# Kernel optimization log

Measured on AMD Instinct MI355X. Metric: run time of the kernel, lower is better.

The kernel has to match this reference:

```python
import jax, jax.numpy as jnp
import numpy as np

B, C, H, W = 8, 96, 56, 56
N = H * W
K = 9
COUT = 2 * C  # 192


def setup_inputs() -> dict:
    key = jax.random.key(0)
    ks = jax.random.split(key, 12)
    s = 0.05
    inp = {
        "x": jax.random.normal(ks[0], (B, C, H, W), jnp.float32),
        "kmap_w": jax.random.normal(ks[1], (C, 500), jnp.float32) * s,
        "kmap_b": jnp.zeros((500,), jnp.float32),
        "kfc_w": jax.random.normal(ks[2], (500, 64), jnp.float32) * s,
        "kfc_b": jnp.zeros((64,), jnp.float32),
        "kmu_w": jax.random.normal(ks[3], (64, 32), jnp.float32) * s,
        "kmu_b": jnp.zeros((32,), jnp.float32),
        "kdec_w": jax.random.normal(ks[4], (32, K), jnp.float32) * s,
        "kdec_b": jnp.zeros((K,), jnp.float32),
        "ec1_w": jax.random.normal(ks[5], (2 * C, C), jnp.float32) * s,
        "ec1_b": jnp.zeros((C,), jnp.float32),
        "ec2_w": jax.random.normal(ks[6], (2 * C, C), jnp.float32) * s,
        "ec2_b": jnp.zeros((C,), jnp.float32),
        "fc_w": jax.random.normal(ks[7], (C, COUT), jnp.float32) * s,
        "fc_b": jnp.zeros((COUT,), jnp.float32),
        "io_w": jax.random.normal(ks[8], (C, COUT), jnp.float32) * s,
        "io_b": jnp.zeros((COUT,), jnp.float32),
        "up_w": jax.random.normal(ks[9], (2 * COUT, COUT), jnp.float32) * s,
        "up_b": jnp.zeros((COUT,), jnp.float32),
    }
    return inp


def reference(x, kmap_w, kmap_b, kfc_w, kfc_b, kmu_w, kmu_b, kdec_w, kdec_b,
              ec1_w, ec1_b, ec2_w, ec2_b, fc_w, fc_b, io_w, io_b, up_w, up_b):
    b, c, h, w = x.shape
    n = h * w
    xf = x.reshape(b, c, n).transpose(0, 2, 1)  # [B, N, C]

    # ---- dense kNN graph (dilation=1, deterministic) ----
    sq = jnp.sum(xf * xf, axis=-1)  # [B, N]
    dist = sq[:, :, None] - 2.0 * jnp.einsum('bnc,bmc->bnm', xf, xf) + sq[:, None, :]
    _, nn_idx = jax.lax.top_k(-dist, K)  # [B, N, K] local neighbor indices

    nodes = xf.reshape(b * n, c)  # flat node features

    # ---- VAE-like K predictor -> per-node kept-degree (non-differentiable) ----
    hK = nodes @ kmap_w + kmap_b
    hK = jax.nn.relu(hK @ kfc_w + kfc_b)
    mu = hK @ kmu_w + kmu_b
    logits = mu @ kdec_w + kdec_b  # [B*N, K]
    k_int = jnp.argmax(logits, axis=1)  # in [0, K-1]

    # edge mask: keep first k_int[i] of node i's K edges
    edge_mask = (jnp.arange(K)[None, :] < k_int[:, None]).reshape(-1)  # [B*N*K]
    emask = edge_mask.astype(nodes.dtype)[:, None]

    # flatten edges with per-batch node offsets (local -> global indices)
    offs = (jnp.arange(b) * n)[:, None, None]
    src = (nn_idx + offs).reshape(-1)              # x_j
    dst = jnp.repeat(jnp.arange(b * n), K)         # x_i (center)

    def edge_conv(feat, wgt, bias):
        xi = feat[dst]
        xj = feat[src]
        msg = jnp.concatenate([xi, xj - xi], axis=-1) @ wgt + bias
        msg = msg * emask  # pruned edges contribute 0 to 'add' aggregation
        return jax.ops.segment_sum(msg, dst, num_segments=b * n)

    h1 = jax.nn.relu(edge_conv(nodes, ec1_w, ec1_b))
    h2 = edge_conv(h1, ec2_w, ec2_b)
    agg = h2 @ fc_w + fc_b                 # EdgeAgg output [B*N, COUT]

    xio = nodes @ io_w + io_b              # inOutFC
    upd = jax.nn.relu(jnp.concatenate([xio, agg], axis=-1) @ up_w + up_b)

    out = upd.reshape(b, n, 2 * c).transpose(0, 2, 1).reshape(b, 2 * c, h, w)
    return out
```

## Files before the change

### kernel.cpp

```cpp
#include <hip/hip_runtime.h>

#define NODES 25088
#define NB 8
#define NPB 3136
#define C 96
#define KNN 9
#define COUT 192
#define MSPLIT 4
#define T12 12
#define NCAND (MSPLIT * T12)

typedef float f32x4 __attribute__((ext_vector_type(4)));
typedef float f32x16 __attribute__((ext_vector_type(16)));
typedef short s16x8 __attribute__((ext_vector_type(8)));

__device__ __forceinline__ unsigned short f2bf(float x) {
  unsigned u = __float_as_uint(x);
  return (unsigned short)((u + 0x7fffu + ((u >> 16) & 1u)) >> 16);
}
__device__ __forceinline__ float bf2f(unsigned short h) {
  return __uint_as_float(((unsigned)h) << 16);
}

__global__ void transpose_kernel(const float* __restrict__ x, float* __restrict__ xf) {
  __shared__ float t[32][33];
  int b = blockIdx.z, ct = blockIdx.y, nt = blockIdx.x;
  int tx = threadIdx.x, ty = threadIdx.y;
  int n0 = nt * 32, c0 = ct * 32;
  const float* xb = x + (size_t)b * C * NPB;
#pragma unroll
  for (int i = 0; i < 4; i++) {
    int c = c0 + ty + i * 8;
    t[ty + i * 8][tx] = xb[(size_t)c * NPB + n0 + tx];
  }
  __syncthreads();
  float* xfb = xf + (size_t)b * NPB * C;
#pragma unroll
  for (int i = 0; i < 4; i++) {
    int n = n0 + ty + i * 8;
    xfb[(size_t)n * C + c0 + tx] = t[tx][ty + i * 8];
  }
}

__global__ void sqsplit_kernel(const float* __restrict__ xf, float* __restrict__ sq,
                               unsigned short* __restrict__ xh,
                               unsigned short* __restrict__ xl) {
  int node = blockIdx.x * 256 + threadIdx.x;
  const float4* r = (const float4*)(xf + (size_t)node * C);
  ushort4* hp = (ushort4*)(xh + (size_t)node * C);
  ushort4* lp = (ushort4*)(xl + (size_t)node * C);
  float s = 0.f;
#pragma unroll
  for (int i = 0; i < 24; i++) {
    float4 v = r[i];
    s += v.x * v.x + v.y * v.y + v.z * v.z + v.w * v.w;
    ushort4 h, l;
    h.x = f2bf(v.x); l.x = f2bf(v.x - bf2f(h.x));
    h.y = f2bf(v.y); l.y = f2bf(v.y - bf2f(h.y));
    h.z = f2bf(v.z); l.z = f2bf(v.z - bf2f(h.z));
    h.w = f2bf(v.w); l.w = f2bf(v.w - bf2f(h.w));
    hp[i] = h;
    lp[i] = l;
  }
  sq[node] = s;
}

__global__ void fold_all_kernel(
    const float* __restrict__ kmap_w, const float* __restrict__ kmap_b,
    const float* __restrict__ kfc_w, const float* __restrict__ kfc_b,
    const float* __restrict__ kmu_w, const float* __restrict__ kmu_b,
    const float* __restrict__ kdec_w, const float* __restrict__ kdec_b,
    const float* __restrict__ ec1_w, const float* __restrict__ ec2_w,
    const float* __restrict__ io_w, const float* __restrict__ io_b,
    const float* __restrict__ fc_w, const float* __restrict__ fc_b,
    const float* __restrict__ up_w, const float* __restrict__ up_b,
    float* __restrict__ WkP, float* __restrict__ bkP, float* __restrict__ WdP,
    float* __restrict__ bdP, float* __restrict__ bPf,
    unsigned short* __restrict__ B1h, unsigned short* __restrict__ B1l,
    unsigned short* __restrict__ B2h, unsigned short* __restrict__ B2l,
    unsigned short* __restrict__ BFh, unsigned short* __restrict__ BFl) {
  __shared__ float sh[4][64];
  int bid = blockIdx.x, tid = threadIdx.x;
  int tx = tid & 63, ty = tid >> 6;
  if (bid < 96) {
    int m = bid;
    float acc = 0.f;
    for (int k = ty; k < 500; k += 4) acc += kmap_w[m * 500 + k] * kfc_w[k * 64 + tx];
    sh[ty][tx] = acc;
    __syncthreads();
    if (ty == 0) WkP[m * 64 + tx] = sh[0][tx] + sh[1][tx] + sh[2][tx] + sh[3][tx];
  } else if (bid == 96) {
    float acc = 0.f;
    for (int k = ty; k < 500; k += 4) acc += kmap_b[k] * kfc_w[k * 64 + tx];
    sh[ty][tx] = acc;
    __syncthreads();
    if (ty == 0) bkP[tx] = sh[0][tx] + sh[1][tx] + sh[2][tx] + sh[3][tx] + kfc_b[tx];
  } else if (bid < 161) {
    int m = bid - 97;
    float acc = 0.f;
    if (tx < 9) {
      for (int k = ty; k < 32; k += 4) acc += kmu_w[m * 32 + k] * kdec_w[k * 9 + tx];
    }
    sh[ty][tx] = acc;
    __syncthreads();
    if (ty == 0 && tx < 9) WdP[m * 9 + tx] = sh[0][tx] + sh[1][tx] + sh[2][tx] + sh[3][tx];
  } else if (bid == 161) {
    float acc = 0.f;
    if (tx < 9) {
      for (int k = ty; k < 32; k += 4) acc += kmu_b[k] * kdec_w[k * 9 + tx];
    }
    sh[ty][tx] = acc;
    __syncthreads();
    if (ty == 0 && tx < 9) bdP[tx] = sh[0][tx] + sh[1][tx] + sh[2][tx] + sh[3][tx] + kdec_b[tx];
  } else if (bid < 234) {
    int t = (bid - 162) * 256 + tid;
    int n = t / 192, k = t % 192;
    float v = ec1_w[(size_t)k * 96 + n];
    if (k < 96) v -= ec1_w[(size_t)(k + 96) * 96 + n];
    unsigned short h = f2bf(v);
    B1h[t] = h;
    B1l[t] = f2bf(v - bf2f(h));
  } else if (bid < 306) {
    int t = (bid - 234) * 256 + tid;
    int n = t / 192, k = t % 192;
    float v = ec2_w[(size_t)k * 96 + n];
    if (k < 96) v -= ec2_w[(size_t)(k + 96) * 96 + n];
    unsigned short h = f2bf(v);
    B2h[t] = h;
    B2l[t] = f2bf(v - bf2f(h));
  } else if (bid < 594) {
    int r = bid - 306;
    int m = r / 3, n = (r % 3) * 64 + tx;
    float acc = 0.f;
    for (int k = ty; k < 192; k += 4) acc += io_w[m * 192 + k] * up_w[(size_t)k * 192 + n];
    sh[ty][tx] = acc;
    __syncthreads();
    if (ty == 0) {
      float v = sh[0][tx] + sh[1][tx] + sh[2][tx] + sh[3][tx];
      unsigned short h = f2bf(v);
      BFh[(size_t)n * 192 + m] = h;
      BFl[(size_t)n * 192 + m] = f2bf(v - bf2f(h));
    }
  } else if (bid < 882) {
    int r = bid - 594;
    int m = r / 3, n = (r % 3) * 64 + tx;
    float acc = 0.f;
    for (int k = ty; k < 192; k += 4)
      acc += fc_w[m * 192 + k] * up_w[(size_t)(192 + k) * 192 + n];
    sh[ty][tx] = acc;
    __syncthreads();
    if (ty == 0) {
      float v = sh[0][tx] + sh[1][tx] + sh[2][tx] + sh[3][tx];
      unsigned short h = f2bf(v);
      BFh[(size_t)n * 192 + 96 + m] = h;
      BFl[(size_t)n * 192 + 96 + m] = f2bf(v - bf2f(h));
    }
  } else {
    if (tid < 192) {
      float acc = up_b[tid];
      for (int k = 0; k < 192; k++) {
        acc += io_b[k] * up_w[k * 192 + tid];
        acc += fc_b[k] * up_w[(192 + k) * 192 + tid];
      }
      bPf[tid] = acc;
    }
  }
}

__global__ __launch_bounds__(256) void gemmhead_kernel(
    const float* __restrict__ A0, const float* __restrict__ B,
    const float* __restrict__ bias, const float* __restrict__ WdP,
    const float* __restrict__ bdP, int* __restrict__ kint,
    float* __restrict__ rs) {
  __shared__ float As[16][68];
  __shared__ float Bs[16][68];
  __shared__ float hs[64][68];
  __shared__ float wd[576];
  __shared__ float bd[9];
  int tid = threadIdx.x;
  int tx = tid & 15, ty = tid >> 4;
  int row0 = blockIdx.x * 64;
  for (int f = tid; f < 576; f += 256) wd[f] = WdP[f];
  if (tid < 9) bd[tid] = bdP[tid];
  float acc[4][4] = {};
  int ai = tid >> 2;
  int ak = (tid & 3) * 4;
  int bk = tid >> 4;
  int bj = (tid & 15) * 4;

  for (int k0 = 0; k0 < 96; k0 += 16) {
    {
      int r = row0 + ai;
      float4 v = *(const float4*)(A0 + (size_t)r * 96 + k0 + ak);
      As[ak + 0][ai] = v.x;
      As[ak + 1][ai] = v.y;
      As[ak + 2][ai] = v.z;
      As[ak + 3][ai] = v.w;
    }
    {
      int kg = k0 + bk;
      float4 v = *(const float4*)(B + (size_t)kg * 64 + bj);
      *(float4*)&Bs[bk][bj] = v;
    }
    __syncthreads();
#pragma unroll
    for (int kk = 0; kk < 16; kk++) {
      float4 av = *(const float4*)&As[kk][ty * 4];
      float4 bv = *(const float4*)&Bs[kk][tx * 4];
      acc[0][0] += av.x * bv.x; acc[0][1] += av.x * bv.y; acc[0][2] += av.x * bv.z; acc[0][3] += av.x * bv.w;
      acc[1][0] += av.y * bv.x; acc[1][1] += av.y * bv.y; acc[1][2] += av.y * bv.z; acc[1][3] += av.y * bv.w;
      acc[2][0] += av.z * bv.x; acc[2][1] += av.z * bv.y; acc[2][2] += av.z * bv.z; acc[2][3] += av.z * bv.w;
      acc[3][0] += av.w * bv.x; acc[3][1] += av.w * bv.y; acc[3][2] += av.w * bv.z; acc[3][3] += av.w * bv.w;
    }
    __syncthreads();
  }
#pragma unroll
  for (int ii = 0; ii < 4; ii++) {
#pragma unroll
    for (int jj = 0; jj < 4; jj++) {
      int j = tx * 4 + jj;
      hs[ty * 4 + ii][j] = fmaxf(acc[ii][jj] + bias[j], 0.f);
    }
  }
  __syncthreads();
  if (tid < 64) {
    int node = row0 + tid;
    const float4* hp = (const float4*)hs[tid];
    float4 h[16];
#pragma unroll
    for (int i = 0; i < 16; i++) h[i] = hp[i];
    float best = -3.4e38f;
    int bi = 0;
#pragma unroll
    for (int n = 0; n < 9; n++) {
      float a = bd[n];
#pragma unroll
      for (int k = 0; k < 16; k++) {
        float4 hv = h[k];
        a += hv.x * wd[(4 * k + 0) * 9 + n] + hv.y * wd[(4 * k + 1) * 9 + n] +
             hv.z * wd[(4 * k + 2) * 9 + n] + hv.w * wd[(4 * k + 3) * 9 + n];
      }
      if (a > best) { best = a; bi = n; }
    }
    kint[node] = bi;
    rs[node] = (float)bi;
  }
}

__device__ __forceinline__ void ce(float& a, float& b) {
  float lo = fminf(a, b);
  b = fmaxf(a, b);
  a = lo;
}

__device__ __forceinline__ void sort16(float* s) {
  ce(s[0], s[1]); ce(s[2], s[3]); ce(s[0], s[2]); ce(s[1], s[3]); ce(s[1], s[2]);
  ce(s[4], s[5]); ce(s[6], s[7]); ce(s[4], s[6]); ce(s[5], s[7]); ce(s[5], s[6]);
  ce(s[0], s[4]); ce(s[1], s[5]); ce(s[2], s[6]); ce(s[3], s[7]);
  ce(s[2], s[4]); ce(s[3], s[5]);
  ce(s[1], s[2]); ce(s[3], s[4]); ce(s[5], s[6]);
  ce(s[8], s[9]); ce(s[10], s[11]); ce(s[8], s[10]); ce(s[9], s[11]); ce(s[9], s[10]);
  ce(s[12], s[13]); ce(s[14], s[15]); ce(s[12], s[14]); ce(s[13], s[15]); ce(s[13], s[14]);
  ce(s[8], s[12]); ce(s[9], s[13]); ce(s[10], s[14]); ce(s[11], s[15]);
  ce(s[10], s[12]); ce(s[11], s[13]);
  ce(s[9], s[10]); ce(s[11], s[12]); ce(s[13], s[14]);
  ce(s[0], s[8]); ce(s[1], s[9]); ce(s[2], s[10]); ce(s[3], s[11]);
  ce(s[4], s[12]); ce(s[5], s[13]); ce(s[6], s[14]); ce(s[7], s[15]);
  ce(s[4], s[8]); ce(s[5], s[9]); ce(s[6], s[10]); ce(s[7], s[11]);
  ce(s[2], s[4]); ce(s[3], s[5]); ce(s[6], s[8]); ce(s[7], s[9]);
  ce(s[10], s[12]); ce(s[11], s[13]);
  ce(s[1], s[2]); ce(s[3], s[4]); ce(s[5], s[6]); ce(s[7], s[8]);
  ce(s[9], s[10]); ce(s[11], s[12]); ce(s[13], s[14]);
}

__device__ __forceinline__ void bmerge12(float* fd, const float* s) {
  float L[12];
#pragma unroll
  for (int i = 0; i < 12; i++) L[i] = fminf(fd[i], s[11 - i]);
  ce(L[0], L[8]); ce(L[1], L[9]); ce(L[2], L[10]); ce(L[3], L[11]);
  ce(L[4], L[8]); ce(L[5], L[9]); ce(L[6], L[10]); ce(L[7], L[11]);
  ce(L[0], L[2]); ce(L[1], L[3]); ce(L[4], L[6]); ce(L[5], L[7]);
  ce(L[8], L[10]); ce(L[9], L[11]);
  ce(L[0], L[1]); ce(L[2], L[3]); ce(L[4], L[5]); ce(L[6], L[7]);
  ce(L[8], L[9]); ce(L[10], L[11]);
#pragma unroll
  for (int i = 0; i < 12; i++) fd[i] = L[i];
}

__global__ __launch_bounds__(256) void knn_mfma_kernel(
    const unsigned short* __restrict__ xh, const unsigned short* __restrict__ xl,
    const float* __restrict__ sq, int* __restrict__ pk_i) {
  __shared__ __align__(16) float smem_f[256 * 17];
  unsigned short* mh = (unsigned short*)smem_f;
  float* sqs = smem_f + 3328;
  int tid = threadIdx.x;
  int lane = tid & 63, wv = tid >> 6;
  int wm = wv >> 1, wq = wv & 1;
  int b = blockIdx.y, z = blockIdx.z;
  int q0 = blockIdx.x * 64;
  int bbase = b * NPB;
  int t0 = (z * 49) / MSPLIT, t1 = ((z + 1) * 49) / MSPLIT;

  int koff = (lane >> 5) * 8;
  int qrow = bbase + q0 + wq * 32 + (lane & 31);
  s16x8 bqh[6], bql[6];
  {
    const unsigned short* ph = xh + (size_t)qrow * 96 + koff;
    const unsigned short* pl = xl + (size_t)qrow * 96 + koff;
#pragma unroll
    for (int kc = 0; kc < 6; kc++) {
      bqh[kc] = *(const s16x8*)(ph + kc * 16);
      bql[kc] = *(const s16x8*)(pl + kc * 16);
    }
  }
  float sqr = sq[qrow];

  float fd[12];
#pragma unroll
  for (int k = 0; k < 12; k++) fd[k] = 3.4e38f;

  int srow = tid >> 2, sseg = tid & 3;
  int soff = srow * 104 + sseg * 24;

  s16x8 st0, st1, st2;
  float stq = 0.f;
  {
    const unsigned short* gh =
        xh + (size_t)(bbase + t0 * 64 + srow) * 96 + sseg * 24;
    st0 = *(const s16x8*)(gh);
    st1 = *(const s16x8*)(gh + 8);
    st2 = *(const s16x8*)(gh + 16);
    if (tid < 64) stq = sq[bbase + t0 * 64 + tid];
  }

  int sqbase = wm * 32 + 4 * (lane >> 5);

  for (int t = t0; t < t1; t++) {
    __syncthreads();
    *(s16x8*)(mh + soff) = st0;
    *(s16x8*)(mh + soff + 8) = st1;
    *(s16x8*)(mh + soff + 16) = st2;
    if (tid < 64) sqs[tid] = stq;
    __syncthreads();

    int tn = (t + 1 < t1) ? (t + 1) : t;
    {
      const unsigned short* gh =
          xh + (size_t)(bbase + tn * 64 + srow) * 96 + sseg * 24;
      st0 = *(const s16x8*)(gh);
      st1 = *(const s16x8*)(gh + 8);
      st2 = *(const s16x8*)(gh + 16);
      if (tid < 64) stq = sq[bbase + tn * 64 + tid];
    }

    int mrow = wm * 32 + (lane & 31);
    f32x16 acc = (f32x16){0.f, 0.f, 0.f, 0.f, 0.f, 0.f, 0.f, 0.f,
                          0.f, 0.f, 0.f, 0.f, 0.f, 0.f, 0.f, 0.f};
#pragma unroll
    for (int kc = 0; kc < 6; kc++) {
      s16x8 amh = *(const s16x8*)(mh + mrow * 104 + kc * 16 + koff);
      acc = __builtin_amdgcn_mfma_f32_32x32x16_bf16(amh, bqh[kc], acc, 0, 0, 0);
      acc = __builtin_amdgcn_mfma_f32_32x32x16_bf16(amh, bql[kc], acc, 0, 0, 0);
    }

    f32x4 sm0 = *(const f32x4*)(sqs + sqbase);
    f32x4 sm1 = *(const f32x4*)(sqs + sqbase + 8);
    f32x4 sm2 = *(const f32x4*)(sqs + sqbase + 16);
    f32x4 sm3 = *(const f32x4*)(sqs + sqbase + 24);

    int lbase = (t - t0) * 64;
    float cs[16];
#pragma unroll
    for (int reg = 0; reg < 16; reg++) {
      int g = reg >> 2, e = reg & 3;
      float sqm = (g == 0) ? sm0[e] : (g == 1) ? sm1[e] : (g == 2) ? sm2[e] : sm3[e];
      int mloc = wm * 32 + e + 8 * g + 4 * (lane >> 5);
      float d = fmaf(-2.f, acc[reg], sqr + sqm);
      unsigned u = (__float_as_uint(d) & 0xFFFFFC00u) | (unsigned)(lbase + mloc);
      cs[reg] = __uint_as_float(u);
    }
    sort16(cs);
    bmerge12(fd, cs);
  }

  __syncthreads();
  float* cd = smem_f;
#pragma unroll
  for (int k = 0; k < 12; k++) cd[(wv * 64 + lane) * 13 + k] = fd[k];
  __syncthreads();
  if (wv == 0) {
    int wva = lane >> 5, ql = lane & 31;
    int ra = wva * 64 + ql, rb = wva * 64 + ql + 32;
    int rc = (wva + 2) * 64 + ql, rd = (wva + 2) * 64 + ql + 32;
    float A[12], B[12];
#pragma unroll
    for (int k = 0; k < 12; k++) { A[k] = cd[ra * 13 + k]; B[k] = cd[rb * 13 + k]; }
    bmerge12(A, B);
    float Cc[12], Dd[12];
#pragma unroll
    for (int k = 0; k < 12; k++) { Cc[k] = cd[rc * 13 + k]; Dd[k] = cd[rd * 13 + k]; }
    bmerge12(Cc, Dd);
    bmerge12(A, Cc);
    size_t base = ((size_t)(bbase + q0 + lane) * MSPLIT + z) * T12;
#pragma unroll
    for (int k = 0; k < T12; k++) {
      int mloc = (int)(__float_as_uint(A[k]) & 0x3FFu) + t0 * 64;
      pk_i[base + k] = bbase + mloc;
    }
  }
}

__global__ __launch_bounds__(256) void rescore_kernel(
    const float* __restrict__ xf, const float* __restrict__ sq,
    const int* __restrict__ pk_i, int* __restrict__ nn) {
  __shared__ float qr[4][96];
  __shared__ float sqq[4];
  int tid = threadIdx.x;
  int qloc = tid >> 6, c = tid & 63;
  int qbase = blockIdx.x * 4;
  for (int f = tid; f < 4 * 96; f += 256)
    qr[f / 96][f % 96] = xf[(size_t)(qbase + f / 96) * 96 + f % 96];
  if (tid < 4) sqq[tid] = sq[qbase + tid];
  __syncthreads();

  int q = qbase + qloc;
  int jv = 0;
  if (c < NCAND) jv = pk_i[(size_t)q * NCAND + c];

  int grp = c >> 3;
  int chunk = c & 7;
  const float4* qp = (const float4*)qr[qloc];
  float4 qv0 = qp[chunk];
  float4 qv1 = qp[chunk + 8];
  float4 qv2 = qp[chunk + 16];

  float dots[6];
#pragma unroll
  for (int it = 0; it < 6; it++) {
    int j = __shfl(jv, it * 8 + grp, 64);
    const float4* mp = (const float4*)(xf + (size_t)j * 96);
    float4 m0 = mp[chunk];
    float4 m1 = mp[chunk + 8];
    float4 m2 = mp[chunk + 16];
    float p = qv0.x * m0.x + qv0.y * m0.y + qv0.z * m0.z + qv0.w * m0.w +
              qv1.x * m1.x + qv1.y * m1.y + qv1.z * m1.z + qv1.w * m1.w +
              qv2.x * m2.x + qv2.y * m2.y + qv2.z * m2.z + qv2.w * m2.w;
    p += __shfl_xor(p, 1, 64);
    p += __shfl_xor(p, 2, 64);
    p += __shfl_xor(p, 4, 64);
    dots[it] = p;
  }

  float g0 = __shfl(dots[0], (c & 7) * 8, 64);
  float g1 = __shfl(dots[1], (c & 7) * 8, 64);
  float g2 = __shfl(dots[2], (c & 7) * 8, 64);
  float g3 = __shfl(dots[3], (c & 7) * 8, 64);
  float g4 = __shfl(dots[4], (c & 7) * 8, 64);
  float g5 = __shfl(dots[5], (c & 7) * 8, 64);
  int itstar = c >> 3;
  float dot = g0;
  dot = (itstar == 1) ? g1 : dot;
  dot = (itstar == 2) ? g2 : dot;
  dot = (itstar == 3) ? g3 : dot;
  dot = (itstar == 4) ? g4 : dot;
  dot = (itstar == 5) ? g5 : dot;

  unsigned long long key = 0xFFFFFFFFFFFFFFFFull;
  if (c < NCAND) {
    float d = (sqq[qloc] - 2.0f * dot) + sq[jv];
    unsigned u = __float_as_uint(d);
    u ^= (u & 0x80000000u) ? 0xFFFFFFFFu : 0x80000000u;
    key = ((unsigned long long)u << 32) | (unsigned)jv;
  }

#pragma unroll
  for (int k = 2; k <= 64; k <<= 1) {
#pragma unroll
    for (int jm = k >> 1; jm >= 1; jm >>= 1) {
      unsigned long long other = __shfl_xor(key, jm, 64);
      bool takeMin = ((c & jm) == 0) == ((c & k) == 0);
      bool sw = (other < key) == takeMin;
      key = sw ? other : key;
    }
  }

  if (c < KNN) {
    nn[(size_t)q * KNN + c] = (int)(unsigned)(key & 0xFFFFFFFFull);
  }
}

__global__ __launch_bounds__(192) void mfma_ec_fused_kernel(
    const unsigned short* __restrict__ A0h, const unsigned short* __restrict__ A0l,
    const float* __restrict__ feat32, const unsigned short* __restrict__ gfh,
    const unsigned short* __restrict__ gfl, int mode,
    const int* __restrict__ nn, const int* __restrict__ kint,
    const unsigned short* __restrict__ Bth, const unsigned short* __restrict__ Btl,
    const float* __restrict__ rs, const float* __restrict__ bias, int relu,
    unsigned short* __restrict__ Oh, unsigned short* __restrict__ Ol) {
  __shared__ float rsL[32];
  __shared__ float bL[96];
  __shared__ __align__(16) unsigned short Sth[32][104];
  __shared__ __align__(16) unsigned short Stl[32][104];
  int tid = threadIdx.x, lane = tid & 63, wv = tid >> 6;
  int m0 = blockIdx.x * 32;
  if (tid < 32) rsL[tid] = rs[m0 + tid];
  if (tid < 96) bL[tid] = bias[tid];

  for (int it = tid; it < 768; it += 192) {
    int nl = it / 24, c4 = it % 24;
    int node = m0 + nl;
    int kc = kint[node];
    const int* nr = nn + (size_t)node * KNN;
    float4 acc = make_float4(0.f, 0.f, 0.f, 0.f);
    if (mode == 0) {
      for (int k = 0; k < kc; k++) {
        int j = nr[k];
        float4 v = ((const float4*)(feat32 + (size_t)j * C))[c4];
        acc.x += v.x; acc.y += v.y; acc.z += v.z; acc.w += v.w;
      }
    } else {
      for (int k = 0; k < kc; k++) {
        int j = nr[k];
        ushort4 h = ((const ushort4*)(gfh + (size_t)j * C))[c4];
        ushort4 l = ((const ushort4*)(gfl + (size_t)j * C))[c4];
        acc.x += bf2f(h.x) + bf2f(l.x);
        acc.y += bf2f(h.y) + bf2f(l.y);
        acc.z += bf2f(h.z) + bf2f(l.z);
        acc.w += bf2f(h.w) + bf2f(l.w);
      }
    }
    ushort4 h, l;
    h.x = f2bf(acc.x); l.x = f2bf(acc.x - bf2f(h.x));
    h.y = f2bf(acc.y); l.y = f2bf(acc.y - bf2f(h.y));
    h.z = f2bf(acc.z); l.z = f2bf(acc.z - bf2f(h.z));
    h.w = f2bf(acc.w); l.w = f2bf(acc.w - bf2f(h.w));
    *(ushort4*)&Sth[nl][c4 * 4] = h;
    *(ushort4*)&Stl[nl][c4 * 4] = l;
  }
  __syncthreads();

  int koff = (lane >> 5) * 8;
  int arow = m0 + (lane & 31);
  const unsigned short* a0h = A0h + (size_t)arow * 96 + koff;
  const unsigned short* a0l = A0l + (size_t)arow * 96 + koff;
  int rloc = lane & 31;
  int n = wv * 32 + (lane & 31);

  f32x16 acc1 = (f32x16){0.f, 0.f, 0.f, 0.f, 0.f, 0.f, 0.f, 0.f,
                         0.f, 0.f, 0.f, 0.f, 0.f, 0.f, 0.f, 0.f};
  f32x16 acc2 = acc1;

#pragma unroll
  for (int c = 0; c < 6; c++) {
    s16x8 ah = *(const s16x8*)(a0h + c * 16);
    s16x8 al = *(const s16x8*)(a0l + c * 16);
    size_t bo = (size_t)n * 192 + c * 16 + koff;
    s16x8 bh = *(const s16x8*)(Bth + bo);
    s16x8 bl = *(const s16x8*)(Btl + bo);
    acc1 = __builtin_amdgcn_mfma_f32_32x32x16_bf16(ah, bh, acc1, 0, 0, 0);
    acc1 = __builtin_amdgcn_mfma_f32_32x32x16_bf16(al, bh, acc1, 0, 0, 0);
    acc1 = __builtin_amdgcn_mfma_f32_32x32x16_bf16(ah, bl, acc1, 0, 0, 0);
  }
#pragma unroll
  for (int c = 6; c < 12; c++) {
    s16x8 ah = *(const s16x8*)(&Sth[rloc][(c - 6) * 16 + koff]);
    s16x8 al = *(const s16x8*)(&Stl[rloc][(c - 6) * 16 + koff]);
    size_t bo = (size_t)n * 192 + c * 16 + koff;
    s16x8 bh = *(const s16x8*)(Bth + bo);
    s16x8 bl = *(const s16x8*)(Btl + bo);
    acc2 = __builtin_amdgcn_mfma_f32_32x32x16_bf16(ah, bh, acc2, 0, 0, 0);
    acc2 = __builtin_amdgcn_mfma_f32_32x32x16_bf16(al, bh, acc2, 0, 0, 0);
    acc2 = __builtin_amdgcn_mfma_f32_32x32x16_bf16(ah, bl, acc2, 0, 0, 0);
  }

  float bn = bL[n];
#pragma unroll
  for (int reg = 0; reg < 16; reg++) {
    int rl = (reg & 3) + 8 * (reg >> 2) + 4 * (lane >> 5);
    int r = m0 + rl;
    float v = rsL[rl] * (acc1[reg] + bn) + acc2[reg];
    if (relu) v = fmaxf(v, 0.f);
    unsigned short h = f2bf(v);
    Oh[(size_t)r * 96 + n] = h;
    Ol[(size_t)r * 96 + n] = f2bf(v - bf2f(h));
  }
}

__global__ __launch_bounds__(192) void mfma_final_kernel(
    const unsigned short* __restrict__ A0h, const unsigned short* __restrict__ A0l,
    const unsigned short* __restrict__ A1h, const unsigned short* __restrict__ A1l,
    const unsigned short* __restrict__ Bth, const unsigned short* __restrict__ Btl,
    const float* __restrict__ bias, float* __restrict__ out) {
  __shared__ float bL[96];
  __shared__ float tt[3][32][33];
  int tid = threadIdx.x, lane = tid & 63, wv = tid >> 6;
  int m0 = blockIdx.x * 32;
  int n0 = blockIdx.y * 96;
  if (tid < 96) bL[tid] = bias[n0 + tid];
  __syncthreads();

  int koff = (lane >> 5) * 8;
  int arow = m0 + (lane & 31);
  const unsigned short* a0h = A0h + (size_t)arow * 96 + koff;
  const unsigned short* a0l = A0l + (size_t)arow * 96 + koff;
  const unsigned short* a1h = A1h + (size_t)arow * 96 + koff;
  const unsigned short* a1l = A1l + (size_t)arow * 96 + koff;
  int nloc = lane & 31;
  int n = n0 + wv * 32 + nloc;

  f32x16 acc = (f32x16){0.f, 0.f, 0.f, 0.f, 0.f, 0.f, 0.f, 0.f,
                        0.f, 0.f, 0.f, 0.f, 0.f, 0.f, 0.f, 0.f};
#pragma unroll
  for (int c = 0; c < 12; c++) {
    s16x8 ah, al;
    if (c < 6) {
      ah = *(const s16x8*)(a0h + c * 16);
      al = *(const s16x8*)(a0l + c * 16);
    } else {
      ah = *(const s16x8*)(a1h + (c - 6) * 16);
      al = *(const s16x8*)(a1l + (c - 6) * 16);
    }
    size_t bo = (size_t)n * 192 + c * 16 + koff;
    s16x8 bh = *(const s16x8*)(Bth + bo);
    s16x8 bl = *(const s16x8*)(Btl + bo);
    acc = __builtin_amdgcn_mfma_f32_32x32x16_bf16(ah, bh, acc, 0, 0, 0);
    acc = __builtin_amdgcn_mfma_f32_32x32x16_bf16(al, bh, acc, 0, 0, 0);
    acc = __builtin_amdgcn_mfma_f32_32x32x16_bf16(ah, bl, acc, 0, 0, 0);
  }

  float bn = bL[wv * 32 + nloc];
#pragma unroll
  for (int reg = 0; reg < 16; reg++) {
    int rl = (reg & 3) + 8 * (reg >> 2) + 4 * (lane >> 5);
    tt[wv][nloc][rl] = fmaxf(acc[reg] + bn, 0.f);
  }
  __builtin_amdgcn_s_waitcnt(0);
  int gbase = m0 + nloc;
  int bb = gbase / NPB, nidx = gbase % NPB;
#pragma unroll
  for (int i = 0; i < 16; i++) {
    int nl = 2 * i + (lane >> 5);
    float v = tt[wv][nl][nloc];
    int ng = n0 + wv * 32 + nl;
    out[(size_t)bb * COUT * NPB + (size_t)ng * NPB + nidx] = v;
  }
}

extern "C" void kernel_launch(void* const* d_in, const int* in_sizes, int n_in,
                              void* d_out, int out_size, void* d_ws, size_t ws_size,
                              hipStream_t stream) {
  const float* x      = (const float*)d_in[0];
  const float* kmap_w = (const float*)d_in[1];
  const float* kmap_b = (const float*)d_in[2];
  const float* kfc_w  = (const float*)d_in[3];
  const float* kfc_b  = (const float*)d_in[4];
  const float* kmu_w  = (const float*)d_in[5];
  const float* kmu_b  = (const float*)d_in[6];
  const float* kdec_w = (const float*)d_in[7];
  const float* kdec_b = (const float*)d_in[8];
  const float* ec1_w  = (const float*)d_in[9];
  const float* ec1_b  = (const float*)d_in[10];
  const float* ec2_w  = (const float*)d_in[11];
  const float* ec2_b  = (const float*)d_in[12];
  const float* fc_w   = (const float*)d_in[13];
  const float* fc_b   = (const float*)d_in[14];
  const float* io_w   = (const float*)d_in[15];
  const float* io_b   = (const float*)d_in[16];
  const float* up_w   = (const float*)d_in[17];
  const float* up_b   = (const float*)d_in[18];

  char* ws = (char*)d_ws;
  size_t off = 0;
  auto alloc = [&](size_t bytes) -> void* {
    void* p = ws + off;
    off += (bytes + 255) & ~(size_t)255;
    return p;
  };
  const size_t HBF = (size_t)NODES * C * 2;
  float* xf   = (float*)alloc((size_t)NODES * C * 4);
  float* sqb  = (float*)alloc((size_t)NODES * 4);
  float* rs   = (float*)alloc((size_t)NODES * 4);
  int*   kint = (int*)alloc((size_t)NODES * 4);
  int*   nn   = (int*)alloc((size_t)NODES * KNN * 4);
  unsigned short* xh = (unsigned short*)alloc(HBF);
  unsigned short* xl = (unsigned short*)alloc(HBF);
  char* region = (char*)alloc((size_t)NODES * COUT * 4);
  int*   pk_i   = (int*)region;
  unsigned short* h1h = (unsigned short*)region;
  unsigned short* h1l = (unsigned short*)(region + HBF);
  unsigned short* h2h = (unsigned short*)(region + 2 * HBF);
  unsigned short* h2l = (unsigned short*)(region + 3 * HBF);
  float* WkP = (float*)alloc(96 * 64 * 4);
  float* bkP = (float*)alloc(64 * 4);
  float* WdP = (float*)alloc(64 * 9 * 4);
  float* bdP = (float*)alloc(16 * 4);
  float* bPf = (float*)alloc(192 * 4);
  unsigned short* B1h = (unsigned short*)alloc(96 * 192 * 2);
  unsigned short* B1l = (unsigned short*)alloc(96 * 192 * 2);
  unsigned short* B2h = (unsigned short*)alloc(96 * 192 * 2);
  unsigned short* B2l = (unsigned short*)alloc(96 * 192 * 2);
  unsigned short* BFh = (unsigned short*)alloc(192 * 192 * 2);
  unsigned short* BFl = (unsigned short*)alloc(192 * 192 * 2);

  transpose_kernel<<<dim3(98, 3, 8), dim3(32, 8), 0, stream>>>(x, xf);
  sqsplit_kernel<<<98, 256, 0, stream>>>(xf, sqb, xh, xl);

  fold_all_kernel<<<883, 256, 0, stream>>>(
      kmap_w, kmap_b, kfc_w, kfc_b, kmu_w, kmu_b, kdec_w, kdec_b, ec1_w, ec2_w,
      io_w, io_b, fc_w, fc_b, up_w, up_b,
      WkP, bkP, WdP, bdP, bPf, B1h, B1l, B2h, B2l, BFh, BFl);

  gemmhead_kernel<<<392, 256, 0, stream>>>(xf, WkP, bkP, WdP, bdP, kint, rs);

  knn_mfma_kernel<<<dim3(49, 8, MSPLIT), 256, 0, stream>>>(xh, xl, sqb, pk_i);
  rescore_kernel<<<6272, 256, 0, stream>>>(xf, sqb, pk_i, nn);

  mfma_ec_fused_kernel<<<784, 192, 0, stream>>>(
      xh, xl, xf, (const unsigned short*)nullptr, (const unsigned short*)nullptr,
      0, nn, kint, B1h, B1l, rs, ec1_b, 1, h1h, h1l);
  mfma_ec_fused_kernel<<<784, 192, 0, stream>>>(
      h1h, h1l, (const float*)nullptr, h1h, h1l,
      1, nn, kint, B2h, B2l, rs, ec2_b, 0, h2h, h2l);
  mfma_final_kernel<<<dim3(784, 2), 192, 0, stream>>>(xh, xl, h2h, h2l, BFh, BFl,
                                                      bPf, (float*)d_out);
}
```

Measured before the change: 338.3 us.

## Fuse transpose with bf16 split and stage two kNN tiles per sync

The transpose kernel and the square-norm/bf16 hi-lo split kernel are merged into one kernel that handles all 96 channels of a 32-node tile in shared memory, so xf no longer has to be written and read back between launches. The kNN kernel now loads two 64-candidate tiles into separate shared buffers per iteration, halving the number of barrier pairs and issuing larger prefetch loads. In exchange, shared-memory use and staging registers in the kNN kernel roughly double, which may lower occupancy. The fused transpose reads shared memory with strided column access, which may cause bank conflicts.

```diff
diff --git a/kernel.cpp b/kernel.cpp
--- a/kernel.cpp
+++ b/kernel.cpp
@@ -22,47 +22,54 @@
   return __uint_as_float(((unsigned)h) << 16);
 }
 
-__global__ void transpose_kernel(const float* __restrict__ x, float* __restrict__ xf) {
-  __shared__ float t[32][33];
-  int b = blockIdx.z, ct = blockIdx.y, nt = blockIdx.x;
-  int tx = threadIdx.x, ty = threadIdx.y;
-  int n0 = nt * 32, c0 = ct * 32;
+__global__ __launch_bounds__(256) void txsq_kernel(
+    const float* __restrict__ x, float* __restrict__ xf, float* __restrict__ sq,
+    unsigned short* __restrict__ xh, unsigned short* __restrict__ xl) {
+  __shared__ float t[96][33];
+  int tid = threadIdx.x;
+  int b = blockIdx.y;
+  int n0 = blockIdx.x * 32;
   const float* xb = x + (size_t)b * C * NPB;
-#pragma unroll
-  for (int i = 0; i < 4; i++) {
-    int c = c0 + ty + i * 8;
-    t[ty + i * 8][tx] = xb[(size_t)c * NPB + n0 + tx];
+  int tn = tid & 31, tc = tid >> 5;
+#pragma unroll
+  for (int i = 0; i < 12; i++) {
+    int c = tc + i * 8;
+    t[c][tn] = xb[(size_t)c * NPB + n0 + tn];
   }
   __syncthreads();
-  float* xfb = xf + (size_t)b * NPB * C;
-#pragma unroll
-  for (int i = 0; i < 4; i++) {
-    int n = n0 + ty + i * 8;
-    xfb[(size_t)n * C + c0 + tx] = t[tx][ty + i * 8];
-  }
-}
-
-__global__ void sqsplit_kernel(const float* __restrict__ xf, float* __restrict__ sq,
-                               unsigned short* __restrict__ xh,
-                               unsigned short* __restrict__ xl) {
-  int node = blockIdx.x * 256 + threadIdx.x;
-  const float4* r = (const float4*)(xf + (size_t)node * C);
-  ushort4* hp = (ushort4*)(xh + (size_t)node * C);
-  ushort4* lp = (ushort4*)(xl + (size_t)node * C);
-  float s = 0.f;
-#pragma unroll
-  for (int i = 0; i < 24; i++) {
-    float4 v = r[i];
-    s += v.x * v.x + v.y * v.y + v.z * v.z + v.w * v.w;
+#pragma unroll
+  for (int k = 0; k < 3; k++) {
+    int it = tid + k * 256;
+    int nl = it / 24, c4 = it % 24;
+    int node = b * NPB + n0 + nl;
+    float4 v;
+    v.x = t[4 * c4 + 0][nl];
+    v.y = t[4 * c4 + 1][nl];
+    v.z = t[4 * c4 + 2][nl];
+    v.w = t[4 * c4 + 3][nl];
     ushort4 h, l;
     h.x = f2bf(v.x); l.x = f2bf(v.x - bf2f(h.x));
     h.y = f2bf(v.y); l.y = f2bf(v.y - bf2f(h.y));
     h.z = f2bf(v.z); l.z = f2bf(v.z - bf2f(h.z));
     h.w = f2bf(v.w); l.w = f2bf(v.w - bf2f(h.w));
-    hp[i] = h;
-    lp[i] = l;
-  }
-  sq[node] = s;
+    ((float4*)(xf + (size_t)node * C))[c4] = v;
+    ((ushort4*)(xh + (size_t)node * C))[c4] = h;
+    ((ushort4*)(xl + (size_t)node * C))[c4] = l;
+  }
+  if (tid < 32) {
+    int node = b * NPB + n0 + tid;
+    float s = 0.f;
+#pragma unroll
+    for (int i = 0; i < 24; i++) {
+      float4 v;
+      v.x = t[4 * i + 0][tid];
+      v.y = t[4 * i + 1][tid];
+      v.z = t[4 * i + 2][tid];
+      v.w = t[4 * i + 3][tid];
+      s += v.x * v.x + v.y * v.y + v.z * v.z + v.w * v.w;
+    }
+    sq[node] = s;
+  }
 }
 
 __global__ void fold_all_kernel(
@@ -290,9 +297,11 @@
 __global__ __launch_bounds__(256) void knn_mfma_kernel(
     const unsigned short* __restrict__ xh, const unsigned short* __restrict__ xl,
     const float* __restrict__ sq, int* __restrict__ pk_i) {
-  __shared__ __align__(16) float smem_f[256 * 17];
-  unsigned short* mh = (unsigned short*)smem_f;
-  float* sqs = smem_f + 3328;
+  __shared__ __align__(16) float smem_f[6784];
+  unsigned short* mhA = (unsigned short*)smem_f;
+  unsigned short* mhB = (unsigned short*)(smem_f + 3328);
+  float* sqsA = smem_f + 6656;
+  float* sqsB = smem_f + 6720;
   int tid = threadIdx.x;
   int lane = tid & 63, wv = tid >> 6;
   int wm = wv >> 1, wq = wv & 1;
@@ -319,68 +328,107 @@
 #pragma unroll
   for (int k = 0; k < 12; k++) fd[k] = 3.4e38f;
 
-  int srow = tid >> 2, sseg = tid & 3;
-  int soff = srow * 104 + sseg * 24;
-
-  s16x8 st0, st1, st2;
+  int srow = tid >> 1;
+  int tloc = srow >> 6;
+  int rrow = srow & 63;
+  int sseg = (tid & 1) * 48;
+  int soff = rrow * 104 + sseg;
+  unsigned short* mhd = tloc ? mhB : mhA;
+
+  s16x8 st[6];
   float stq = 0.f;
   {
-    const unsigned short* gh =
-        xh + (size_t)(bbase + t0 * 64 + srow) * 96 + sseg * 24;
-    st0 = *(const s16x8*)(gh);
-    st1 = *(const s16x8*)(gh + 8);
-    st2 = *(const s16x8*)(gh + 16);
-    if (tid < 64) stq = sq[bbase + t0 * 64 + tid];
+    int tA = t0 + tloc;
+    int ts = (tA < t1) ? tA : (t1 - 1);
+    const unsigned short* gh = xh + (size_t)(bbase + ts * 64 + rrow) * 96 + sseg;
+#pragma unroll
+    for (int i = 0; i < 6; i++) st[i] = *(const s16x8*)(gh + i * 8);
+    if (tid < 128) {
+      int tq = t0 + (tid >> 6);
+      int tqs = (tq < t1) ? tq : (t1 - 1);
+      stq = sq[bbase + tqs * 64 + (tid & 63)];
+    }
   }
 
   int sqbase = wm * 32 + 4 * (lane >> 5);
-
-  for (int t = t0; t < t1; t++) {
-    __syncthreads();
-    *(s16x8*)(mh + soff) = st0;
-    *(s16x8*)(mh + soff + 8) = st1;
-    *(s16x8*)(mh + soff + 16) = st2;
-    if (tid < 64) sqs[tid] = stq;
-    __syncthreads();
-
-    int tn = (t + 1 < t1) ? (t + 1) : t;
+  int mrow = wm * 32 + (lane & 31);
+  int np = (t1 - t0 + 1) >> 1;
+
+  for (int p = 0; p < np; p++) {
+    int ta = t0 + 2 * p, tb = ta + 1;
+    __syncthreads();
+#pragma unroll
+    for (int i = 0; i < 6; i++) *(s16x8*)(mhd + soff + i * 8) = st[i];
+    if (tid < 128) ((tid >> 6) ? sqsB : sqsA)[tid & 63] = stq;
+    __syncthreads();
+
     {
-      const unsigned short* gh =
-          xh + (size_t)(bbase + tn * 64 + srow) * 96 + sseg * 24;
-      st0 = *(const s16x8*)(gh);
-      st1 = *(const s16x8*)(gh + 8);
-      st2 = *(const s16x8*)(gh + 16);
-      if (tid < 64) stq = sq[bbase + tn * 64 + tid];
-    }
-
-    int mrow = wm * 32 + (lane & 31);
-    f32x16 acc = (f32x16){0.f, 0.f, 0.f, 0.f, 0.f, 0.f, 0.f, 0.f,
-                          0.f, 0.f, 0.f, 0.f, 0.f, 0.f, 0.f, 0.f};
-#pragma unroll
-    for (int kc = 0; kc < 6; kc++) {
-      s16x8 amh = *(const s16x8*)(mh + mrow * 104 + kc * 16 + koff);
-      acc = __builtin_amdgcn_mfma_f32_32x32x16_bf16(amh, bqh[kc], acc, 0, 0, 0);
-      acc = __builtin_amdgcn_mfma_f32_32x32x16_bf16(amh, bql[kc], acc, 0, 0, 0);
-    }
-
-    f32x4 sm0 = *(const f32x4*)(sqs + sqbase);
-    f32x4 sm1 = *(const f32x4*)(sqs + sqbase + 8);
-    f32x4 sm2 = *(const f32x4*)(sqs + sqbase + 16);
-    f32x4 sm3 = *(const f32x4*)(sqs + sqbase + 24);
-
-    int lbase = (t - t0) * 64;
-    float cs[16];
-#pragma unroll
-    for (int reg = 0; reg < 16; reg++) {
-      int g = reg >> 2, e = reg & 3;
-      float sqm = (g == 0) ? sm0[e] : (g == 1) ? sm1[e] : (g == 2) ? sm2[e] : sm3[e];
-      int mloc = wm * 32 + e + 8 * g + 4 * (lane >> 5);
-      float d = fmaf(-2.f, acc[reg], sqr + sqm);
-      unsigned u = (__float_as_uint(d) & 0xFFFFFC00u) | (unsigned)(lbase + mloc);
-      cs[reg] = __uint_as_float(u);
-    }
-    sort16(cs);
-    bmerge12(fd, cs);
+      int tn = t0 + 2 * (p + 1) + tloc;
+      int ts = (tn < t1) ? tn : (t1 - 1);
+      const unsigned short* gh = xh + (size_t)(bbase + ts * 64 + rrow) * 96 + sseg;
+#pragma unroll
+      for (int i = 0; i < 6; i++) st[i] = *(const s16x8*)(gh + i * 8);
+      if (tid < 128) {
+        int tq = t0 + 2 * (p + 1) + (tid >> 6);
+        int tqs = (tq < t1) ? tq : (t1 - 1);
+        stq = sq[bbase + tqs * 64 + (tid & 63)];
+      }
+    }
+
+    {
+      f32x16 acc = (f32x16){0.f, 0.f, 0.f, 0.f, 0.f, 0.f, 0.f, 0.f,
+                            0.f, 0.f, 0.f, 0.f, 0.f, 0.f, 0.f, 0.f};
+#pragma unroll
+      for (int kc = 0; kc < 6; kc++) {
+        s16x8 amh = *(const s16x8*)(mhA + mrow * 104 + kc * 16 + koff);
+        acc = __builtin_amdgcn_mfma_f32_32x32x16_bf16(amh, bqh[kc], acc, 0, 0, 0);
+        acc = __builtin_amdgcn_mfma_f32_32x32x16_bf16(amh, bql[kc], acc, 0, 0, 0);
+      }
+      f32x4 sm0 = *(const f32x4*)(sqsA + sqbase);
+      f32x4 sm1 = *(const f32x4*)(sqsA + sqbase + 8);
+      f32x4 sm2 = *(const f32x4*)(sqsA + sqbase + 16);
+      f32x4 sm3 = *(const f32x4*)(sqsA + sqbase + 24);
+      int lbase = (ta - t0) * 64;
+      float cs[16];
+#pragma unroll
+      for (int reg = 0; reg < 16; reg++) {
+        int g = reg >> 2, e = reg & 3;
+        float sqm = (g == 0) ? sm0[e] : (g == 1) ? sm1[e] : (g == 2) ? sm2[e] : sm3[e];
+        int mloc = wm * 32 + e + 8 * g + 4 * (lane >> 5);
+        float d = fmaf(-2.f, acc[reg], sqr + sqm);
+        unsigned u = (__float_as_uint(d) & 0xFFFFFC00u) | (unsigned)(lbase + mloc);
+        cs[reg] = __uint_as_float(u);
+      }
+      sort16(cs);
+      bmerge12(fd, cs);
+    }
+    if (tb < t1) {
+      f32x16 acc = (f32x16){0.f, 0.f, 0.f, 0.f, 0.f, 0.f, 0.f, 0.f,
+                            0.f, 0.f, 0.f, 0.f, 0.f, 0.f, 0.f, 0.f};
+#pragma unroll
+      for (int kc = 0; kc < 6; kc++) {
+        s16x8 amh = *(const s16x8*)(mhB + mrow * 104 + kc * 16 + koff);
+        acc = __builtin_amdgcn_mfma_f32_32x32x16_bf16(amh, bqh[kc], acc, 0, 0, 0);
+        acc = __builtin_amdgcn_mfma_f32_32x32x16_bf16(amh, bql[kc], acc, 0, 0, 0);
+      }
+      f32x4 sm0 = *(const f32x4*)(sqsB + sqbase);
+      f32x4 sm1 = *(const f32x4*)(sqsB + sqbase + 8);
+      f32x4 sm2 = *(const f32x4*)(sqsB + sqbase + 16);
+      f32x4 sm3 = *(const f32x4*)(sqsB + sqbase + 24);
+      int lbase = (tb - t0) * 64;
+      float cs[16];
+#pragma unroll
+      for (int reg = 0; reg < 16; reg++) {
+        int g = reg >> 2, e = reg & 3;
+        float sqm = (g == 0) ? sm0[e] : (g == 1) ? sm1[e] : (g == 2) ? sm2[e] : sm3[e];
+        int mloc = wm * 32 + e + 8 * g + 4 * (lane >> 5);
+        float d = fmaf(-2.f, acc[reg], sqr + sqm);
+        unsigned u = (__float_as_uint(d) & 0xFFFFFC00u) | (unsigned)(lbase + mloc);
+        cs[reg] = __uint_as_float(u);
+      }
+      sort16(cs);
+      bmerge12(fd, cs);
+    }
   }
 
   __syncthreads();
@@ -702,8 +750,7 @@
   unsigned short* BFh = (unsigned short*)alloc(192 * 192 * 2);
   unsigned short* BFl = (unsigned short*)alloc(192 * 192 * 2);
 
-  transpose_kernel<<<dim3(98, 3, 8), dim3(32, 8), 0, stream>>>(x, xf);
-  sqsplit_kernel<<<98, 256, 0, stream>>>(xf, sqb, xh, xl);
+  txsq_kernel<<<dim3(98, 8), 256, 0, stream>>>(x, xf, sqb, xh, xl);
 
   fold_all_kernel<<<883, 256, 0, stream>>>(
       kmap_w, kmap_b, kfc_w, kfc_b, kmu_w, kmu_b, kdec_w, kdec_b, ec1_w, ec2_w,
```

New measurement: 329.2 us. -2.7%, faster.
